# Performance work log

Measured on AMD Instinct MI355X. Metric: run time of the kernel, lower is better.

## Reference

```python
import jax, jax.numpy as jnp
import numpy as np


def _bilinear(plane, coords):
    # plane: [B, C, H, W]; coords: [B, N, 2] in [-1, 1]; coords[...,0]->x (W axis), [...,1]->y (H axis)
    # matches F.grid_sample(mode='bilinear', padding_mode='border', align_corners=True)
    B, C, H, W = plane.shape
    x = jnp.clip((coords[..., 0] + 1.0) * 0.5 * (W - 1), 0.0, W - 1)
    y = jnp.clip((coords[..., 1] + 1.0) * 0.5 * (H - 1), 0.0, H - 1)
    x0 = jnp.floor(x)
    y0 = jnp.floor(y)
    x0i = x0.astype(jnp.int32)
    y0i = y0.astype(jnp.int32)
    x1i = jnp.minimum(x0i + 1, W - 1)
    y1i = jnp.minimum(y0i + 1, H - 1)
    wx = (x - x0)[:, :, None]
    wy = (y - y0)[:, :, None]
    pf = plane.reshape(B, C, H * W)

    def g(yi, xi):
        idx = (yi * W + xi)[:, None, :]            # [B,1,N]
        return jnp.take_along_axis(pf, idx, axis=2).transpose(0, 2, 1)  # [B,N,C]

    f00 = g(y0i, x0i)
    f01 = g(y0i, x1i)
    f10 = g(y1i, x0i)
    f11 = g(y1i, x1i)
    return (f00 * (1 - wx) * (1 - wy) + f01 * wx * (1 - wy)
            + f10 * (1 - wx) * wy + f11 * wx * wy)


def _sample(p, c_xz, c_xy, c_yz):
    # project 3D points onto the three canonical planes and sum bilinear features
    return (_bilinear(c_xz, p[..., jnp.array([0, 2])])
            + _bilinear(c_xy, p[..., jnp.array([0, 1])])
            + _bilinear(c_yz, p[..., jnp.array([1, 2])]))


def setup_inputs() -> dict:
    key = jax.random.key(0)
    ks = jax.random.split(key, 10)
    B, N, C, S, H = 8, 4096, 128, 8, 64
    query_pos = jax.random.uniform(ks[0], (B, N, 3), dtype=jnp.float32) * 2.0 - 1.0
    c_xz = jax.random.normal(ks[1], (B, C, H, H), dtype=jnp.float32)
    c_xy = jax.random.normal(ks[2], (B, C, H, H), dtype=jnp.float32)
    c_yz = jax.random.normal(ks[3], (B, C, H, H), dtype=jnp.float32)
    s = C ** -0.5
    Wq = jax.random.normal(ks[4], (C, C), dtype=jnp.float32) * s
    Wk = jax.random.normal(ks[5], (C, C), dtype=jnp.float32) * s
    Wv = jax.random.normal(ks[6], (C, C), dtype=jnp.float32) * s
    Wout = jax.random.normal(ks[7], (C, C), dtype=jnp.float32) * s
    Woff = jax.random.normal(ks[8], (C, 3 * S), dtype=jnp.float32) * s * 0.1  # small offsets
    return dict(query_pos=query_pos, c_xz=c_xz, c_xy=c_xy, c_yz=c_yz,
                Wq=Wq, bq=jnp.zeros((C,), jnp.float32),
                Wk=Wk, bk=jnp.zeros((C,), jnp.float32),
                Wv=Wv, bv=jnp.zeros((C,), jnp.float32),
                Wout=Wout, bout=jnp.zeros((C,), jnp.float32),
                Woff=Woff, boff=jnp.zeros((3 * S,), jnp.float32))


def reference(query_pos, c_xz, c_xy, c_yz, Wq, bq, Wk, bk, Wv, bv,
              Wout, bout, Woff, boff):
    B, N, _ = query_pos.shape
    C = Wq.shape[0]
    S = Woff.shape[1] // 3
    # sample features at query points (bilinear gather from triplanes)
    feature = _sample(query_pos, c_xz, c_xy, c_yz)                     # [B,N,C]
    # learned deformable offsets -> S auxiliary sample points per query
    offset = (feature @ Woff + boff).reshape(B, N, S, 3)
    aux_pts = offset + query_pos[:, :, None, :]                        # [B,N,S,3]
    aux_feat = _sample(aux_pts.reshape(B, N * S, 3),
                       c_xz, c_xy, c_yz).reshape(B, N, S, C)           # [B,N,S,C]
    k = aux_feat @ Wk + bk                                             # [B,N,S,C]
    v = aux_feat @ Wv + bv
    q = feature @ Wq + bq                                              # [B,N,C]
    scale = C ** (-0.5)
    q = q / scale  # faithful to original: q = q / self.scale
    sim = jnp.einsum('bnd,bnjd->bnj', q, k)                            # [B,N,S]
    attn = jax.nn.softmax(sim, axis=-1)
    out = jnp.einsum('bnj,bnjd->bnd', attn, v)                         # [B,N,C]
    out = out @ Wout + bout + feature                                  # residual
    return out
```

## Files before the change

### kernel.cpp

```cpp
#include <hip/hip_runtime.h>
#include <math.h>

#define BB 8
#define NN 4096
#define CC 128
#define SS 8
#define HH 64
#define HW 4096
#define PLANE_B (HW*CC)
#define SQRT_C 11.3137084989847603904f

__global__ __launch_bounds__(128) void transpose_planes(
    const float* __restrict__ pxz, const float* __restrict__ pxy,
    const float* __restrict__ pyz, float* __restrict__ dst) {
  int bid = blockIdx.x;
  int c   = threadIdx.x;
  int hw0 = (bid & 255) * 16;
  int b   = (bid >> 8) & 7;
  int p   = bid >> 11;
  const float* src = (p == 0) ? pxz : (p == 1) ? pxy : pyz;
  const float4* s4 = (const float4*)(src + (size_t)(b * CC + c) * HW + hw0);
  float4 v0 = s4[0], v1 = s4[1], v2 = s4[2], v3 = s4[3];
  float vals[16];
  vals[0]=v0.x; vals[1]=v0.y; vals[2]=v0.z; vals[3]=v0.w;
  vals[4]=v1.x; vals[5]=v1.y; vals[6]=v1.z; vals[7]=v1.w;
  vals[8]=v2.x; vals[9]=v2.y; vals[10]=v2.z; vals[11]=v2.w;
  vals[12]=v3.x; vals[13]=v3.y; vals[14]=v3.z; vals[15]=v3.w;
  float* d = dst + (size_t)(p * BB + b) * PLANE_B + (size_t)hw0 * CC + c;
#pragma unroll
  for (int i = 0; i < 16; ++i) d[i * CC] = vals[i];
}

__global__ __launch_bounds__(128) void prep_mats(
    const float* __restrict__ Wq, const float* __restrict__ bq,
    const float* __restrict__ Wk,
    const float* __restrict__ Wv, const float* __restrict__ bv,
    const float* __restrict__ Wout, const float* __restrict__ bout,
    const float* __restrict__ Woff,
    float* __restrict__ Mt, float* __restrict__ u,
    float* __restrict__ W2, float* __restrict__ b2,
    float* __restrict__ Wofft) {
  int t = threadIdx.x;
  int blk = blockIdx.x;
  if (blk < 128) {
    __shared__ float lwq[128];
    lwq[t] = Wq[blk * 128 + t];
    __syncthreads();
    float acc = 0.f;
#pragma unroll 8
    for (int d = 0; d < 128; ++d) acc += Wk[t * 128 + d] * lwq[d];
    Mt[blk * 128 + t] = SQRT_C * acc;
  } else if (blk < 256) {
    int c = blk - 128;
    float acc = 0.f;
#pragma unroll 8
    for (int e = 0; e < 128; ++e) acc += Wv[c * 128 + e] * Wout[e * 128 + t];
    W2[c * 128 + t] = acc;
  } else if (blk == 256) {
    float au = 0.f, ab = 0.f;
    for (int d = 0; d < 128; ++d) au += Wk[t * 128 + d] * bq[d];
    u[t] = SQRT_C * au;
    for (int e = 0; e < 128; ++e) ab += bv[e] * Wout[e * 128 + t];
    b2[t] = ab + bout[t];
  } else {
#pragma unroll
    for (int j = 0; j < 24; ++j) Wofft[j * 128 + t] = Woff[t * 24 + j];
  }
}

__device__ __forceinline__ void make_combo(float cx, float cy,
                                           int4* oi, float4* ow) {
  float fx = fminf(fmaxf((cx + 1.f) * 31.5f, 0.f), 63.f);
  float fy = fminf(fmaxf((cy + 1.f) * 31.5f, 0.f), 63.f);
  float x0f = floorf(fx), y0f = floorf(fy);
  int x0 = (int)x0f, y0 = (int)y0f;
  int x1 = min(x0 + 1, 63), y1 = min(y0 + 1, 63);
  float wx = fx - x0f, wy = fy - y0f;
  int r0 = y0 << 15, r1 = y1 << 15;
  int cb0 = x0 << 9, cb1 = x1 << 9;
  *oi = make_int4(r0 + cb0, r0 + cb1, r1 + cb0, r1 + cb1);
  float wxy = wx * wy;
  *ow = make_float4(1.f - wx - wy + wxy, wx - wxy, wy - wxy, wxy);
}

__device__ __forceinline__ float ldf(const char* p, int off) {
  return *(const float*)(p + off);
}

__global__ __launch_bounds__(128, 4) void deform_attn7(
    const float* __restrict__ qpos, const float* __restrict__ pT,
    const float* __restrict__ Mt, const float* __restrict__ u,
    const float* __restrict__ W2, const float* __restrict__ bias2,
    const float* __restrict__ Wofft, const float* __restrict__ boff,
    float* __restrict__ out) {
  const int tid = threadIdx.x;
  const int c = tid;
  const int l = tid & 63;
  const int wv = tid >> 6;
  const int bid = blockIdx.x;
  const int b = bid & 7;
  const int n0 = (bid >> 3) * 8;

  __shared__ float spos[24];
  __shared__ int4   sfi[24];
  __shared__ float4 sfw[24];
  __shared__ int4   sci[192];
  __shared__ float4 scw[192];
  __shared__ __align__(16) float sbuf[CC * 8];
  __shared__ float soff[8][24];
  __shared__ float sred[8][2][8];

  if (tid < 24) spos[tid] = qpos[(size_t)(b * NN + n0) * 3 + tid];
  __syncthreads();

  const char* pb0 = (const char*)(pT + (size_t)(0 * BB + b) * PLANE_B + c);
  const char* pb1 = (const char*)(pT + (size_t)(1 * BB + b) * PLANE_B + c);
  const char* pb2 = (const char*)(pT + (size_t)(2 * BB + b) * PLANE_B + c);

  if (tid < 24) {
    int p = tid >> 3, q = tid & 7;
    float px = spos[q * 3 + 0], py = spos[q * 3 + 1], pz = spos[q * 3 + 2];
    float cx = (p == 2) ? py : px;
    float cy = (p == 1) ? py : pz;
    make_combo(cx, cy, &sfi[tid], &sfw[tid]);
  }
  __syncthreads();

  float featr[8];
#pragma unroll
  for (int q = 0; q < 8; ++q) {
    float f = 0.f;
#pragma unroll
    for (int p = 0; p < 3; ++p) {
      int4 oi = sfi[p * 8 + q];
      float4 w = sfw[p * 8 + q];
      const char* base = (p == 0) ? pb0 : (p == 1) ? pb1 : pb2;
      f += w.x * ldf(base, oi.x) + w.y * ldf(base, oi.y)
         + w.z * ldf(base, oi.z) + w.w * ldf(base, oi.w);
    }
    featr[q] = f;
    sbuf[c * 8 + q] = f;
  }
  __syncthreads();

  float qk[8];
  {
    float uc = u[c];
#pragma unroll
    for (int q = 0; q < 8; ++q) qk[q] = uc;
#pragma unroll 4
    for (int cp = 0; cp < CC; ++cp) {
      float m = Mt[cp * CC + c];
      float4 f0 = *(const float4*)&sbuf[cp * 8];
      float4 f1 = *(const float4*)&sbuf[cp * 8 + 4];
      qk[0] += m * f0.x; qk[1] += m * f0.y; qk[2] += m * f0.z; qk[3] += m * f0.w;
      qk[4] += m * f1.x; qk[5] += m * f1.y; qk[6] += m * f1.z; qk[7] += m * f1.w;
    }
  }

#pragma unroll
  for (int rep = 0; rep < 2; ++rep) {
    int m = rep * 128 + tid;
    if (m < 192) {
      int q = m / 24;
      int t24 = m - q * 24;
      float acc = boff[t24];
      const float* wrow = Wofft + t24 * 128;
#pragma unroll 4
      for (int cp = 0; cp < CC; ++cp) acc += sbuf[cp * 8 + q] * wrow[cp];
      soff[q][t24] = acc;
    }
  }
  __syncthreads();

#pragma unroll
  for (int rep = 0; rep < 2; ++rep) {
    int m = rep * 128 + tid;
    if (m < 192) {
      int p = m >> 6, q = (m >> 3) & 7, j = m & 7;
      float ox = spos[q * 3 + 0] + soff[q][j * 3 + 0];
      float oy = spos[q * 3 + 1] + soff[q][j * 3 + 1];
      float oz = spos[q * 3 + 2] + soff[q][j * 3 + 2];
      float cx = (p == 2) ? oy : ox;
      float cy = (p == 1) ? oy : oz;
      make_combo(cx, cy, &sci[m], &scw[m]);
    }
  }
  __syncthreads();

  const int lb0 = l & 1, lb1 = (l >> 1) & 1, lb2 = (l >> 2) & 1;
#pragma unroll
  for (int q = 0; q < 8; ++q) {
    float a8[8], part[8];
#pragma unroll
    for (int j = 0; j < 8; ++j) {
      float a = 0.f;
#pragma unroll
      for (int p = 0; p < 3; ++p) {
        int idx = p * 64 + q * 8 + j;
        int4 oi = sci[idx];
        float4 w = scw[idx];
        const char* base = (p == 0) ? pb0 : (p == 1) ? pb1 : pb2;
        a += w.x * ldf(base, oi.x) + w.y * ldf(base, oi.y)
           + w.z * ldf(base, oi.z) + w.w * ldf(base, oi.w);
      }
      a8[j] = a;
      part[j] = a * qk[q];
    }
    float s2[4];
#pragma unroll
    for (int k = 0; k < 4; ++k) {
      float pa = part[2 * k], pb_ = part[2 * k + 1];
      float snd = lb0 ? pa : pb_;
      float kp  = lb0 ? pb_ : pa;
      s2[k] = kp + __shfl_xor(snd, 1);
    }
    float s4[2];
#pragma unroll
    for (int k = 0; k < 2; ++k) {
      float pa = s2[2 * k], pb_ = s2[2 * k + 1];
      float snd = lb1 ? pa : pb_;
      float kp  = lb1 ? pb_ : pa;
      s4[k] = kp + __shfl_xor(snd, 2);
    }
    float s8;
    {
      float snd = lb2 ? s4[0] : s4[1];
      float kp  = lb2 ? s4[1] : s4[0];
      s8 = kp + __shfl_xor(snd, 4);
    }
    s8 += __shfl_xor(s8, 8);
    s8 += __shfl_xor(s8, 16);
    s8 += __shfl_xor(s8, 32);
    if (l < 8) sred[q][wv][l] = s8;
    __syncthreads();
    float sim[8];
#pragma unroll
    for (int j = 0; j < 8; ++j) sim[j] = sred[q][0][j] + sred[q][1][j];
    float mx = fmaxf(fmaxf(fmaxf(sim[0], sim[1]), fmaxf(sim[2], sim[3])),
                     fmaxf(fmaxf(sim[4], sim[5]), fmaxf(sim[6], sim[7])));
    float den = 0.f;
#pragma unroll
    for (int j = 0; j < 8; ++j) { sim[j] = __expf(sim[j] - mx); den += sim[j]; }
    float inv = 1.f / den;
    float w = 0.f;
#pragma unroll
    for (int j = 0; j < 8; ++j) w += sim[j] * a8[j];
    sbuf[c * 8 + q] = w * inv;
  }
  __syncthreads();

  float o[8];
  {
    float bb = bias2[c];
#pragma unroll
    for (int q = 0; q < 8; ++q) o[q] = bb;
#pragma unroll 4
    for (int cp = 0; cp < CC; ++cp) {
      float m = W2[cp * CC + c];
      float4 f0 = *(const float4*)&sbuf[cp * 8];
      float4 f1 = *(const float4*)&sbuf[cp * 8 + 4];
      o[0] += m * f0.x; o[1] += m * f0.y; o[2] += m * f0.z; o[3] += m * f0.w;
      o[4] += m * f1.x; o[5] += m * f1.y; o[6] += m * f1.z; o[7] += m * f1.w;
    }
  }
#pragma unroll
  for (int q = 0; q < 8; ++q) {
    out[(size_t)(b * NN + n0 + q) * CC + c] = o[q] + featr[q];
  }
}

__device__ __forceinline__ float bil(const float* __restrict__ base,
                                     float cx, float cy, int es, int rs) {
  float fx = fminf(fmaxf((cx + 1.f) * 31.5f, 0.f), 63.f);
  float fy = fminf(fmaxf((cy + 1.f) * 31.5f, 0.f), 63.f);
  float x0f = floorf(fx), y0f = floorf(fy);
  int x0 = (int)x0f, y0 = (int)y0f;
  int x1 = min(x0 + 1, 63), y1 = min(y0 + 1, 63);
  float wx = fx - x0f, wy = fy - y0f;
  const float* r0 = base + y0 * rs;
  const float* r1 = base + y1 * rs;
  float f00 = r0[x0 * es], f01 = r0[x1 * es];
  float f10 = r1[x0 * es], f11 = r1[x1 * es];
  float top = f00 + (f01 - f00) * wx;
  float bot = f10 + (f11 - f10) * wx;
  return top + (bot - top) * wy;
}

__global__ __launch_bounds__(128) void deform_attn_fb(
    const float* __restrict__ qpos,
    const float* __restrict__ pxz, const float* __restrict__ pxy,
    const float* __restrict__ pyz,
    const float* __restrict__ Mt, const float* __restrict__ u,
    const float* __restrict__ W2, const float* __restrict__ b2,
    const float* __restrict__ Woff, const float* __restrict__ boff,
    float* __restrict__ out) {
  const int tid = threadIdx.x;
  const int c = tid;
  const int bid = blockIdx.x;
  const int b = bid & 7;
  const int n0 = (bid >> 3) * 8;
  const int es = 1, rs = HH;
  const float* bxz = pxz + (size_t)(b * CC + c) * HW;
  const float* bxy = pxy + (size_t)(b * CC + c) * HW;
  const float* byz = pyz + (size_t)(b * CC + c) * HW;

  __shared__ __align__(16) float sfeat[CC * 8];
  __shared__ __align__(16) float swv[CC * 8];
  __shared__ float spos[24];
  __shared__ float soff[8][24];
  __shared__ float sred[8][2][8];

  if (tid < 24) spos[tid] = qpos[(size_t)(b * NN + n0) * 3 + tid];
  __syncthreads();
#pragma unroll
  for (int q = 0; q < 8; ++q) {
    float px = spos[q*3+0], py = spos[q*3+1], pz = spos[q*3+2];
    sfeat[c*8+q] = bil(bxz,px,pz,es,rs)+bil(bxy,px,py,es,rs)+bil(byz,py,pz,es,rs);
  }
  __syncthreads();
  float qk[8];
  {
    float uc = u[c];
#pragma unroll
    for (int q = 0; q < 8; ++q) qk[q] = uc;
    for (int cp = 0; cp < CC; ++cp) {
      float m = Mt[cp*CC+c];
#pragma unroll
      for (int q = 0; q < 8; ++q) qk[q] += m * sfeat[cp*8+q];
    }
  }
  if (tid < 120) {
    int q = tid/24, j = tid%24;
    float acc = boff[j];
    for (int cp = 0; cp < CC; ++cp) acc += sfeat[cp*8+q]*Woff[cp*24+j];
    soff[q][j] = acc;
  }
  if (tid < 72) {
    int q = 5+tid/24, j = tid%24;
    float acc = boff[j];
    for (int cp = 0; cp < CC; ++cp) acc += sfeat[cp*8+q]*Woff[cp*24+j];
    soff[q][j] = acc;
  }
  __syncthreads();
  const int wvid = tid >> 6;
  for (int q = 0; q < 8; ++q) {
    float px = spos[q*3+0], py = spos[q*3+1], pz = spos[q*3+2];
    float a8[8];
#pragma unroll
    for (int j = 0; j < 8; ++j) {
      float ox = px+soff[q][j*3+0], oy = py+soff[q][j*3+1], oz = pz+soff[q][j*3+2];
      float a = bil(bxz,ox,oz,es,rs)+bil(bxy,ox,oy,es,rs)+bil(byz,oy,oz,es,rs);
      a8[j] = a;
      float p = a * qk[q];
#pragma unroll
      for (int m = 1; m < 64; m <<= 1) p += __shfl_xor(p, m);
      if ((tid & 63) == 0) sred[q][wvid][j] = p;
    }
    __syncthreads();
    float attn[8], mx = -INFINITY;
#pragma unroll
    for (int j = 0; j < 8; ++j) { attn[j] = sred[q][0][j]+sred[q][1][j]; mx = fmaxf(mx, attn[j]); }
    float den = 0.f;
#pragma unroll
    for (int j = 0; j < 8; ++j) { attn[j] = __expf(attn[j]-mx); den += attn[j]; }
    float inv = 1.f/den, w = 0.f;
#pragma unroll
    for (int j = 0; j < 8; ++j) w += attn[j]*a8[j];
    swv[c*8+q] = w*inv;
  }
  __syncthreads();
  float o[8];
  {
    float bb = b2[c];
#pragma unroll
    for (int q = 0; q < 8; ++q) o[q] = bb;
    for (int cp = 0; cp < CC; ++cp) {
      float wv2 = W2[cp*CC+c];
#pragma unroll
      for (int q = 0; q < 8; ++q) o[q] += wv2 * swv[cp*8+q];
    }
  }
#pragma unroll
  for (int q = 0; q < 8; ++q)
    out[(size_t)(b*NN+n0+q)*CC+c] = o[q] + sfeat[c*8+q];
}

extern "C" void kernel_launch(void* const* d_in, const int* in_sizes, int n_in,
                              void* d_out, int out_size, void* d_ws, size_t ws_size,
                              hipStream_t stream) {
  const float* qpos = (const float*)d_in[0];
  const float* pxz  = (const float*)d_in[1];
  const float* pxy  = (const float*)d_in[2];
  const float* pyz  = (const float*)d_in[3];
  const float* Wq   = (const float*)d_in[4];
  const float* bq   = (const float*)d_in[5];
  const float* Wk   = (const float*)d_in[6];
  const float* Wv   = (const float*)d_in[8];
  const float* bv   = (const float*)d_in[9];
  const float* Wout = (const float*)d_in[10];
  const float* bout = (const float*)d_in[11];
  const float* Woff = (const float*)d_in[12];
  const float* boff = (const float*)d_in[13];
  float* out = (float*)d_out;

  float* w = (float*)d_ws;
  const size_t nT = (size_t)3 * BB * HW * CC;
  const size_t matFloats = 16384 + 128 + 16384 + 128 + 24 * 128;
  bool tp = ws_size >= (nT + matFloats) * sizeof(float);

  float* wsT  = w;
  float* wsMt = tp ? (w + nT) : w;
  float* wsU  = wsMt + 16384;
  float* wsW2 = wsU + 128;
  float* wsB2 = wsW2 + 16384;
  float* wsWofft = wsB2 + 128;

  prep_mats<<<258, 128, 0, stream>>>(Wq, bq, Wk, Wv, bv, Wout, bout, Woff,
                                     wsMt, wsU, wsW2, wsB2, wsWofft);
  if (tp) {
    transpose_planes<<<3 * BB * (HW / 16), 128, 0, stream>>>(pxz, pxy, pyz, wsT);
    deform_attn7<<<(BB * NN) / 8, 128, 0, stream>>>(
        qpos, wsT, wsMt, wsU, wsW2, wsB2, wsWofft, boff, out);
  } else {
    deform_attn_fb<<<(BB * NN) / 8, 128, 0, stream>>>(
        qpos, pxz, pxy, pyz, wsMt, wsU, wsW2, wsB2, Woff, boff, out);
  }
}
```

Before: 210.7 us.

## Sort queries by Morton cell so blocks gather spatially-local triplane texels

Adds a per-batch counting-sort kernel that buckets query points into an 8x8x8 Morton-ordered grid and writes a permutation. The main attention kernel then processes queries in that sorted order, loading positions and scattering outputs through the index. The aim is that the 8 queries in a block, and neighbouring blocks, touch nearby plane texels, which should improve L2 and cache hit rates on the bilinear gathers. The cost is an extra small kernel launch, indirect position loads, and scattered output writes.

```diff
diff --git a/kernel.cpp b/kernel.cpp
--- a/kernel.cpp
+++ b/kernel.cpp
@@ -29,6 +29,56 @@
   float* d = dst + (size_t)(p * BB + b) * PLANE_B + (size_t)hw0 * CC + c;
 #pragma unroll
   for (int i = 0; i < 16; ++i) d[i * CC] = vals[i];
+}
+
+__device__ __forceinline__ int morton3_3(int cx, int cy, int cz) {
+  int m = 0;
+#pragma unroll
+  for (int k = 0; k < 3; ++k) {
+    m |= ((cx >> k) & 1) << (3 * k);
+    m |= ((cy >> k) & 1) << (3 * k + 1);
+    m |= ((cz >> k) & 1) << (3 * k + 2);
+  }
+  return m;
+}
+
+__global__ __launch_bounds__(1024) void sort_queries(
+    const float* __restrict__ qpos, int* __restrict__ sidx) {
+  const int b = blockIdx.x;
+  const int t = threadIdx.x;
+  __shared__ unsigned short scell[NN];
+  __shared__ int hist[512];
+  __shared__ int tmp[512];
+  __shared__ int cur[512];
+  if (t < 512) hist[t] = 0;
+  __syncthreads();
+  for (int i = t; i < NN; i += 1024) {
+    const float* qp = qpos + ((size_t)b * NN + i) * 3;
+    float x = qp[0], y = qp[1], z = qp[2];
+    int cx = min(7, max(0, (int)((x + 1.f) * 4.f)));
+    int cy = min(7, max(0, (int)((y + 1.f) * 4.f)));
+    int cz = min(7, max(0, (int)((z + 1.f) * 4.f)));
+    int cell = morton3_3(cx, cy, cz);
+    scell[i] = (unsigned short)cell;
+    atomicAdd(&hist[cell], 1);
+  }
+  __syncthreads();
+  if (t < 512) tmp[t] = hist[t];
+  __syncthreads();
+  for (int off = 1; off < 512; off <<= 1) {
+    int v = 0;
+    if (t < 512 && t >= off) v = tmp[t - off];
+    __syncthreads();
+    if (t < 512) tmp[t] += v;
+    __syncthreads();
+  }
+  if (t < 512) cur[t] = tmp[t] - hist[t];
+  __syncthreads();
+  for (int i = t; i < NN; i += 1024) {
+    int cell = scell[i];
+    int pos = atomicAdd(&cur[cell], 1);
+    sidx[b * NN + pos] = i;
+  }
 }
 
 __global__ __launch_bounds__(128) void prep_mats(
@@ -87,8 +137,9 @@
   return *(const float*)(p + off);
 }
 
-__global__ __launch_bounds__(128, 4) void deform_attn7(
-    const float* __restrict__ qpos, const float* __restrict__ pT,
+__global__ __launch_bounds__(128, 4) void deform_attn9(
+    const float* __restrict__ qpos, const int* __restrict__ sidx,
+    const float* __restrict__ pT,
     const float* __restrict__ Mt, const float* __restrict__ u,
     const float* __restrict__ W2, const float* __restrict__ bias2,
     const float* __restrict__ Wofft, const float* __restrict__ boff,
@@ -101,6 +152,7 @@
   const int b = bid & 7;
   const int n0 = (bid >> 3) * 8;
 
+  __shared__ int snidx[8];
   __shared__ float spos[24];
   __shared__ int4   sfi[24];
   __shared__ float4 sfw[24];
@@ -110,7 +162,12 @@
   __shared__ float soff[8][24];
   __shared__ float sred[8][2][8];
 
-  if (tid < 24) spos[tid] = qpos[(size_t)(b * NN + n0) * 3 + tid];
+  if (tid < 8) snidx[tid] = sidx[b * NN + n0 + tid];
+  __syncthreads();
+  if (tid < 24) {
+    int q = tid / 3, comp = tid - q * 3;
+    spos[tid] = qpos[((size_t)b * NN + snidx[q]) * 3 + comp];
+  }
   __syncthreads();
 
   const char* pb0 = (const char*)(pT + (size_t)(0 * BB + b) * PLANE_B + c);
@@ -266,7 +323,7 @@
   }
 #pragma unroll
   for (int q = 0; q < 8; ++q) {
-    out[(size_t)(b * NN + n0 + q) * CC + c] = o[q] + featr[q];
+    out[((size_t)b * NN + snidx[q]) * CC + c] = o[q] + featr[q];
   }
 }
 
@@ -407,7 +464,8 @@
   float* w = (float*)d_ws;
   const size_t nT = (size_t)3 * BB * HW * CC;
   const size_t matFloats = 16384 + 128 + 16384 + 128 + 24 * 128;
-  bool tp = ws_size >= (nT + matFloats) * sizeof(float);
+  const size_t sidxInts = (size_t)BB * NN;
+  bool tp = ws_size >= (nT + matFloats + sidxInts) * sizeof(float);
 
   float* wsT  = w;
   float* wsMt = tp ? (w + nT) : w;
@@ -415,13 +473,15 @@
   float* wsW2 = wsU + 128;
   float* wsB2 = wsW2 + 16384;
   float* wsWofft = wsB2 + 128;
+  int*   wsSidx  = (int*)(wsWofft + 24 * 128);
 
   prep_mats<<<258, 128, 0, stream>>>(Wq, bq, Wk, Wv, bv, Wout, bout, Woff,
                                      wsMt, wsU, wsW2, wsB2, wsWofft);
   if (tp) {
+    sort_queries<<<BB, 1024, 0, stream>>>(qpos, wsSidx);
     transpose_planes<<<3 * BB * (HW / 16), 128, 0, stream>>>(pxz, pxy, pyz, wsT);
-    deform_attn7<<<(BB * NN) / 8, 128, 0, stream>>>(
-        qpos, wsT, wsMt, wsU, wsW2, wsB2, wsWofft, boff, out);
+    deform_attn9<<<(BB * NN) / 8, 128, 0, stream>>>(
+        qpos, wsSidx, wsT, wsMt, wsU, wsW2, wsB2, wsWofft, boff, out);
   } else {
     deform_attn_fb<<<(BB * NN) / 8, 128, 0, stream>>>(
         qpos, pxz, pxy, pyz, wsMt, wsU, wsW2, wsB2, Woff, boff, out);
```

Result: faster. 202.6 us, median of 2 (-3.8%).
